# Performance work log

Measured on AMD Instinct MI355X. Metric: run time of the kernel, lower is better.

The kernel has to match this reference:

```python
import jax, jax.numpy as jnp
import numpy as np
from jax import lax

N_CHANNELS = 16
FIRE_RATE = 0.5
ALIVE_THRESH = 0.1


def _perceive_kernel(n_channels):
    sx = jnp.array([[-1., 0., 1.], [-2., 0., 2.], [-1., 0., 1.]], dtype=jnp.float32) / 8.0
    sy = sx.T
    ident = jnp.outer(jnp.array([0., 1., 0.], jnp.float32), jnp.array([0., 1., 0.], jnp.float32))
    base = jnp.stack([ident, sx, sy], axis=0)            # (3,3,3)
    k = jnp.tile(base, (n_channels, 1, 1))[:, None]       # (3n,1,3,3) order: id,sx,sy per channel
    return k


def _maxpool3(a):
    # torch max_pool2d(kernel=3, stride=1, padding=1) with -inf padding
    return lax.reduce_window(a, -jnp.inf, lax.max, (1, 1, 3, 3), (1, 1, 1, 1),
                             ((0, 0), (0, 0), (1, 1), (1, 1)))


def _living(x):
    return _maxpool3(x[:, 3:4]) > ALIVE_THRESH


def setup_inputs() -> dict:
    key = jax.random.key(0)
    k1, k2, k3, k4, k5 = jax.random.split(key, 5)
    B, C, H, W = 32, N_CHANNELS, 256, 256
    HID = 128
    x = jax.random.uniform(k1, (B, C, H, W), dtype=jnp.float32)
    update_rand = jax.random.uniform(k2, (B, 1, H, W), dtype=jnp.float32)
    w1 = jax.random.normal(k3, (HID, 3 * C), dtype=jnp.float32) * 0.1
    b1 = jax.random.normal(k4, (HID,), dtype=jnp.float32) * 0.1
    w2 = jax.random.normal(k5, (C, HID), dtype=jnp.float32) * 0.1
    return {"x": x, "update_rand": update_rand, "w1": w1, "b1": b1, "w2": w2}


def reference(x, update_rand, w1, b1, w2):
    kernel = _perceive_kernel(N_CHANNELS)
    begin_living = _living(x)                                        # (B,1,H,W) bool
    # depthwise perception: groups = n_channels, 3 filters per group
    y = lax.conv_general_dilated(x, kernel, (1, 1), ((1, 1), (1, 1)),
                                 feature_group_count=N_CHANNELS,
                                 dimension_numbers=("NCHW", "OIHW", "NCHW"))  # (B,3C,H,W)
    h = jax.nn.relu(jnp.einsum("bchw,oc->bohw", y, w1) + b1[None, :, None, None])
    dx = jnp.einsum("bhij,oh->boij", h, w2)                          # (B,C,H,W)
    update = (update_rand <= FIRE_RATE).astype(x.dtype)              # (B,1,H,W)
    x_new = x + dx * update
    alive = begin_living & _living(x_new)
    return x_new * alive.astype(x.dtype)
```

## Files before the change

### kernel.cpp

```cpp
#include <hip/hip_runtime.h>

#define CN 16
#define HN 128
#define IMH 256
#define IMW 256
#define HW (IMH * IMW)

typedef __attribute__((ext_vector_type(8))) short short8;
typedef __attribute__((ext_vector_type(4))) float float4v;
typedef __attribute__((ext_vector_type(2))) unsigned int uint2v;
typedef __attribute__((ext_vector_type(4))) unsigned int uint4v;

__device__ __forceinline__ unsigned int f2bf(float f) {
    unsigned int u = __builtin_bit_cast(unsigned int, f);
    u += 0x7FFFu + ((u >> 16) & 1u);
    return u >> 16;
}
__device__ __forceinline__ unsigned int pack2(float a, float b) {
    unsigned int r;
    asm("v_cvt_pk_bf16_f32 %0, %1, %2" : "=v"(r) : "v"(a), "v"(b));
    return r;
}

__global__ void nca_prep(const float* __restrict__ w1, const float* __restrict__ b1,
                         const float* __restrict__ w2,
                         unsigned short* __restrict__ a1f, unsigned short* __restrict__ b2f)
{
    int t = blockIdx.x * 256 + threadIdx.x;
    if (t < 8192) {
        int j = t & 7, lane = (t >> 3) & 63, ks = (t >> 9) & 1, mi = t >> 10;
        int hid = 16 * mi + (lane & 15);
        int k = 32 * ks + 8 * (lane >> 4) + j;
        float v = 0.f;
        if (k < 48) v = w1[hid * 48 + k];
        else if (k == 48) v = b1[hid];
        a1f[t] = (unsigned short)f2bf(v);
    }
    if (t < 2048) {
        int j = t & 7, lane = (t >> 3) & 63, ks = t >> 9;
        b2f[t] = (unsigned short)f2bf(w2[(lane & 15) * HN + 32 * ks + 8 * (lane >> 4) + j]);
    }
}

__global__ __launch_bounds__(256, 4) void nca_mfma(
    const float* __restrict__ x, const float* __restrict__ upd,
    const unsigned short* __restrict__ a1f, const unsigned short* __restrict__ b2f,
    float* __restrict__ out, float* __restrict__ xn3, unsigned char* __restrict__ bm)
{
    __shared__ __align__(16) union {
        float sx[6][16][34];
        unsigned short hb[4][16][128];
    } u;
    __shared__ __align__(16) unsigned short ybuf[128][64];
    __shared__ __align__(16) float xcT[16][128];

    const int b   = blockIdx.z;
    const int i0  = blockIdx.y * 4;
    const int j0  = blockIdx.x * 32;
    const int tid = threadIdx.x;
    const int lane = tid & 63, w = tid >> 6;
    const int l15 = lane & 15, q = lane >> 4;
    const float* xb = x + (size_t)b * CN * HW;

    short8 a1[8][2];
#pragma unroll
    for (int mi = 0; mi < 8; ++mi)
#pragma unroll
        for (int ks = 0; ks < 2; ++ks)
            a1[mi][ks] = *(const short8*)(a1f + ((mi * 2 + ks) * 64 + lane) * 8);
    short8 b2[4];
#pragma unroll
    for (int ks = 0; ks < 4; ++ks)
        b2[ks] = *(const short8*)(b2f + (ks * 64 + lane) * 8);

    const bool interior = (blockIdx.y > 0) & (blockIdx.y < 63) & (blockIdx.x > 0) & (blockIdx.x < 7);
    {
        const int col = tid & 31;
        if (interior) {
            const float* src = xb + (i0 - 1) * IMW + (j0 - 1);
#pragma unroll
            for (int rt = tid >> 5; rt < 96; rt += 8)
                u.sx[rt >> 4][rt & 15][col] = src[(rt & 15) * HW + (rt >> 4) * IMW + col];
            if (tid < 192) {
                int rt = tid >> 1, col2 = 32 + (tid & 1);
                u.sx[rt >> 4][rt & 15][col2] = src[(rt & 15) * HW + (rt >> 4) * IMW + col2];
            }
        } else {
#pragma unroll
            for (int rt = tid >> 5; rt < 96; rt += 8) {
                int rr = rt >> 4, c = rt & 15;
                int gi = i0 + rr - 1, gj = j0 + col - 1;
                float v = 0.f;
                if ((unsigned)gi < IMH && (unsigned)gj < IMW) v = xb[c * HW + gi * IMW + gj];
                u.sx[rr][c][col] = v;
            }
            if (tid < 192) {
                int rt = tid >> 1, col2 = 32 + (tid & 1);
                int rr = rt >> 4, c = rt & 15;
                int gi = i0 + rr - 1, gj = j0 + col2 - 1;
                float v = 0.f;
                if ((unsigned)gi < IMH && (unsigned)gj < IMW) v = xb[c * HW + gi * IMW + gj];
                u.sx[rr][c][col2] = v;
            }
        }
    }
    __syncthreads();

    const int pix = tid & 127;
    const int ty  = pix >> 5, tx = pix & 31;
    const int cb  = (tid >> 7) << 3;
    float v[24];
#pragma unroll
    for (int c8 = 0; c8 < 8; ++c8) {
        const int c = cb + c8;
        float a00 = u.sx[ty][c][tx],     a01 = u.sx[ty][c][tx + 1],     a02 = u.sx[ty][c][tx + 2];
        float a10 = u.sx[ty + 1][c][tx], a11 = u.sx[ty + 1][c][tx + 1], a12 = u.sx[ty + 1][c][tx + 2];
        float a20 = u.sx[ty + 2][c][tx], a21 = u.sx[ty + 2][c][tx + 1], a22 = u.sx[ty + 2][c][tx + 2];
        v[3 * c8]     = a11;
        v[3 * c8 + 1] = ((a02 - a00) + 2.f * (a12 - a10) + (a22 - a20)) * 0.125f;
        v[3 * c8 + 2] = ((a20 - a00) + 2.f * (a21 - a01) + (a22 - a02)) * 0.125f;
        xcT[c][pix ^ ((c & 7) << 2)] = a11;
        if (cb == 0 && c8 == 3) {
            float m0 = fmaxf(fmaxf(fmaxf(a00, a01), fmaxf(a02, a10)),
                             fmaxf(fmaxf(a11, a12), fmaxf(fmaxf(a20, a21), a22)));
            bm[(size_t)b * HW + (i0 + ty) * IMW + (j0 + tx)] = (m0 > 0.1f) ? 1 : 0;
        }
    }
    {
        unsigned int* yrow = (unsigned int*)&ybuf[pix][0];
        const int gbase = (cb >> 3) * 3;
        const int sw = pix & 7;
#pragma unroll
        for (int t = 0; t < 3; ++t) {
            uint4v g;
#pragma unroll
            for (int k = 0; k < 4; ++k) g[k] = pack2(v[8 * t + 2 * k], v[8 * t + 2 * k + 1]);
            *(uint4v*)&yrow[((gbase + t) ^ sw) << 2] = g;
        }
        if (cb == 8) {
            uint4v g6 = {0x3F80u, 0u, 0u, 0u};
            uint4v g7 = {};
            *(uint4v*)&yrow[(6 ^ sw) << 2] = g6;
            *(uint4v*)&yrow[(7 ^ sw) << 2] = g7;
        }
    }
    __syncthreads();

    const float* ub = upd + (size_t)b * HW;
    float* ob = out + (size_t)b * CN * HW;
    float* n3 = xn3 + (size_t)b * HW;
#pragma unroll
    for (int half = 0; half < 2; ++half) {
        const int nt  = 2 * w + half;
        const int row = 16 * nt + l15;
        const unsigned short* yr = &ybuf[row][0];
        const int rsw = row & 7;
        short8 y0 = *(const short8*)(yr + ((q ^ rsw) << 3));
        short8 y1 = *(const short8*)(yr + (((4 + q) ^ rsw) << 3));
        const int hsw = l15 & 7;
#pragma unroll
        for (int mi = 0; mi < 8; ++mi) {
            float4v acc = {};
            acc = __builtin_amdgcn_mfma_f32_16x16x32_bf16(a1[mi][0], y0, acc, 0, 0, 0);
            acc = __builtin_amdgcn_mfma_f32_16x16x32_bf16(a1[mi][1], y1, acc, 0, 0, 0);
            uint2v hp;
            hp[0] = pack2(fmaxf(acc[0], 0.f), fmaxf(acc[1], 0.f));
            hp[1] = pack2(fmaxf(acc[2], 0.f), fmaxf(acc[3], 0.f));
            *(uint2v*)&u.hb[w][l15][(((2 * mi + (q >> 1)) ^ hsw) << 3) + ((q & 1) << 2)] = hp;
        }
        float4v acc2 = {};
#pragma unroll
        for (int ks = 0; ks < 4; ++ks) {
            short8 hf = *(const short8*)&u.hb[w][l15][((4 * ks + q) ^ hsw) << 3];
            acc2 = __builtin_amdgcn_mfma_f32_16x16x32_bf16(hf, b2[ks], acc2, 0, 0, 0);
        }
        const int i  = i0 + (nt >> 1);
        const int jb = j0 + ((nt & 1) << 4) + (q << 2);
        float4v xc4 = *(const float4v*)&xcT[l15][(16 * nt + 4 * q) ^ ((l15 & 7) << 2)];
        float4v u4  = *(const float4v*)(ub + i * IMW + jb);
        float4v o;
#pragma unroll
        for (int r = 0; r < 4; ++r)
            o[r] = fmaf(acc2[r], (u4[r] <= 0.5f) ? 1.f : 0.f, xc4[r]);
        *(float4v*)(ob + l15 * HW + i * IMW + jb) = o;
        if (l15 == 3) *(float4v*)(n3 + i * IMW + jb) = o;
    }
}

__global__ __launch_bounds__(256) void nca_pass2(
    const float* __restrict__ xn3, const unsigned char* __restrict__ bm,
    float* __restrict__ out)
{
    __shared__ float s[10][130];
    const int b  = blockIdx.z;
    const int i0 = blockIdx.y * 8;
    const int j0 = blockIdx.x * 128;
    const int tid = threadIdx.x;
    const float* n3 = xn3 + (size_t)b * HW;

    for (int idx = tid; idx < 10 * 130; idx += 256) {
        int r = idx / 130, c = idx - r * 130;
        int gi = i0 + r - 1, gj = j0 + c - 1;
        s[r][c] = ((unsigned)gi < IMH && (unsigned)gj < IMW) ? n3[gi * IMW + gj] : -1e30f;
    }
    __syncthreads();

    const int c = tid & 127, rh = (tid >> 7) * 4;
    const unsigned char* bmp = bm + (size_t)b * HW + (i0 + rh) * IMW + (j0 + c);
    float* ob = out + (size_t)b * CN * HW;
#pragma unroll
    for (int k = 0; k < 4; ++k) {
        const int r = rh + k;
        float m = fmaxf(fmaxf(fmaxf(s[r][c], s[r][c + 1]), fmaxf(s[r][c + 2], s[r + 1][c])),
                        fmaxf(fmaxf(s[r + 1][c + 1], s[r + 1][c + 2]),
                              fmaxf(fmaxf(s[r + 2][c], s[r + 2][c + 1]), s[r + 2][c + 2])));
        if (!((m > 0.1f) && bmp[k * IMW])) {
            const int i = i0 + r, j = j0 + c;
#pragma unroll
            for (int ch = 0; ch < CN; ++ch)
                ob[ch * HW + i * IMW + j] = 0.f;
        }
    }
}

extern "C" void kernel_launch(void* const* d_in, const int* in_sizes, int n_in,
                              void* d_out, int out_size, void* d_ws, size_t ws_size,
                              hipStream_t stream) {
    const float* x   = (const float*)d_in[0];
    const float* upd = (const float*)d_in[1];
    const float* w1  = (const float*)d_in[2];
    const float* b1  = (const float*)d_in[3];
    const float* w2  = (const float*)d_in[4];
    float* out = (float*)d_out;

    char* ws = (char*)d_ws;
    float* xn3          = (float*)ws;
    unsigned char* bmp  = (unsigned char*)(ws + (8u << 20));
    unsigned short* a1f = (unsigned short*)(ws + (10u << 20));
    unsigned short* b2f = a1f + 8192;

    nca_prep<<<32, 256, 0, stream>>>(w1, b1, w2, a1f, b2f);
    nca_mfma<<<dim3(8, 64, 32), 256, 0, stream>>>(x, upd, a1f, b2f, out, xn3, bmp);
    nca_pass2<<<dim3(2, 32, 32), 256, 0, stream>>>(xn3, bmp, out);
}
```

Measured before the change: 412.6 us.

## Make MFMA kernel persistent over row strips with register-prefetched halo loads

```diff
diff --git a/kernel.cpp b/kernel.cpp
--- a/kernel.cpp
+++ b/kernel.cpp
@@ -55,12 +55,14 @@
     __shared__ __align__(16) float xcT[16][128];
 
     const int b   = blockIdx.z;
-    const int i0  = blockIdx.y * 4;
     const int j0  = blockIdx.x * 32;
     const int tid = threadIdx.x;
     const int lane = tid & 63, w = tid >> 6;
     const int l15 = lane & 15, q = lane >> 4;
     const float* xb = x + (size_t)b * CN * HW;
+    const float* ub = upd + (size_t)b * HW;
+    float* ob = out + (size_t)b * CN * HW;
+    float* n3 = xn3 + (size_t)b * HW;
 
     short8 a1[8][2];
 #pragma unroll
@@ -73,117 +75,144 @@
     for (int ks = 0; ks < 4; ++ks)
         b2[ks] = *(const short8*)(b2f + (ks * 64 + lane) * 8);
 
-    const bool interior = (blockIdx.y > 0) & (blockIdx.y < 63) & (blockIdx.x > 0) & (blockIdx.x < 7);
-    {
-        const int col = tid & 31;
-        if (interior) {
+    const int col    = tid & 31;
+    const int rbase  = tid >> 5;
+    const int ex_rt  = tid >> 1;
+    const int ex_col = 32 + (tid & 1);
+    const bool xin = (blockIdx.x > 0) & (blockIdx.x < 7);
+
+    float sreg[12];
+    float sx1 = 0.f;
+
+    auto issue_stage = [&](int i0) {
+        if (xin && (i0 > 0) && (i0 < 252)) {
             const float* src = xb + (i0 - 1) * IMW + (j0 - 1);
 #pragma unroll
-            for (int rt = tid >> 5; rt < 96; rt += 8)
-                u.sx[rt >> 4][rt & 15][col] = src[(rt & 15) * HW + (rt >> 4) * IMW + col];
-            if (tid < 192) {
-                int rt = tid >> 1, col2 = 32 + (tid & 1);
-                u.sx[rt >> 4][rt & 15][col2] = src[(rt & 15) * HW + (rt >> 4) * IMW + col2];
-            }
+            for (int k = 0; k < 12; ++k) {
+                const int rt = rbase + 8 * k;
+                sreg[k] = src[(rt & 15) * HW + (rt >> 4) * IMW + col];
+            }
+            if (tid < 192) sx1 = src[(ex_rt & 15) * HW + (ex_rt >> 4) * IMW + ex_col];
         } else {
 #pragma unroll
-            for (int rt = tid >> 5; rt < 96; rt += 8) {
-                int rr = rt >> 4, c = rt & 15;
-                int gi = i0 + rr - 1, gj = j0 + col - 1;
+            for (int k = 0; k < 12; ++k) {
+                const int rt = rbase + 8 * k;
+                const int rr = rt >> 4, c = rt & 15;
+                const int gi = i0 + rr - 1, gj = j0 + col - 1;
                 float v = 0.f;
                 if ((unsigned)gi < IMH && (unsigned)gj < IMW) v = xb[c * HW + gi * IMW + gj];
-                u.sx[rr][c][col] = v;
+                sreg[k] = v;
             }
             if (tid < 192) {
-                int rt = tid >> 1, col2 = 32 + (tid & 1);
-                int rr = rt >> 4, c = rt & 15;
-                int gi = i0 + rr - 1, gj = j0 + col2 - 1;
+                const int rr = ex_rt >> 4, c = ex_rt & 15;
+                const int gi = i0 + rr - 1, gj = j0 + ex_col - 1;
                 float v = 0.f;
                 if ((unsigned)gi < IMH && (unsigned)gj < IMW) v = xb[c * HW + gi * IMW + gj];
-                u.sx[rr][c][col2] = v;
-            }
-        }
-    }
-    __syncthreads();
-
-    const int pix = tid & 127;
-    const int ty  = pix >> 5, tx = pix & 31;
-    const int cb  = (tid >> 7) << 3;
-    float v[24];
-#pragma unroll
-    for (int c8 = 0; c8 < 8; ++c8) {
-        const int c = cb + c8;
-        float a00 = u.sx[ty][c][tx],     a01 = u.sx[ty][c][tx + 1],     a02 = u.sx[ty][c][tx + 2];
-        float a10 = u.sx[ty + 1][c][tx], a11 = u.sx[ty + 1][c][tx + 1], a12 = u.sx[ty + 1][c][tx + 2];
-        float a20 = u.sx[ty + 2][c][tx], a21 = u.sx[ty + 2][c][tx + 1], a22 = u.sx[ty + 2][c][tx + 2];
-        v[3 * c8]     = a11;
-        v[3 * c8 + 1] = ((a02 - a00) + 2.f * (a12 - a10) + (a22 - a20)) * 0.125f;
-        v[3 * c8 + 2] = ((a20 - a00) + 2.f * (a21 - a01) + (a22 - a02)) * 0.125f;
-        xcT[c][pix ^ ((c & 7) << 2)] = a11;
-        if (cb == 0 && c8 == 3) {
-            float m0 = fmaxf(fmaxf(fmaxf(a00, a01), fmaxf(a02, a10)),
-                             fmaxf(fmaxf(a11, a12), fmaxf(fmaxf(a20, a21), a22)));
-            bm[(size_t)b * HW + (i0 + ty) * IMW + (j0 + tx)] = (m0 > 0.1f) ? 1 : 0;
-        }
-    }
-    {
-        unsigned int* yrow = (unsigned int*)&ybuf[pix][0];
-        const int gbase = (cb >> 3) * 3;
-        const int sw = pix & 7;
-#pragma unroll
-        for (int t = 0; t < 3; ++t) {
-            uint4v g;
-#pragma unroll
-            for (int k = 0; k < 4; ++k) g[k] = pack2(v[8 * t + 2 * k], v[8 * t + 2 * k + 1]);
-            *(uint4v*)&yrow[((gbase + t) ^ sw) << 2] = g;
-        }
-        if (cb == 8) {
-            uint4v g6 = {0x3F80u, 0u, 0u, 0u};
-            uint4v g7 = {};
-            *(uint4v*)&yrow[(6 ^ sw) << 2] = g6;
-            *(uint4v*)&yrow[(7 ^ sw) << 2] = g7;
-        }
-    }
-    __syncthreads();
-
-    const float* ub = upd + (size_t)b * HW;
-    float* ob = out + (size_t)b * CN * HW;
-    float* n3 = xn3 + (size_t)b * HW;
-#pragma unroll
-    for (int half = 0; half < 2; ++half) {
-        const int nt  = 2 * w + half;
-        const int row = 16 * nt + l15;
-        const unsigned short* yr = &ybuf[row][0];
-        const int rsw = row & 7;
-        short8 y0 = *(const short8*)(yr + ((q ^ rsw) << 3));
-        short8 y1 = *(const short8*)(yr + (((4 + q) ^ rsw) << 3));
-        const int hsw = l15 & 7;
-#pragma unroll
-        for (int mi = 0; mi < 8; ++mi) {
-            float4v acc = {};
-            acc = __builtin_amdgcn_mfma_f32_16x16x32_bf16(a1[mi][0], y0, acc, 0, 0, 0);
-            acc = __builtin_amdgcn_mfma_f32_16x16x32_bf16(a1[mi][1], y1, acc, 0, 0, 0);
-            uint2v hp;
-            hp[0] = pack2(fmaxf(acc[0], 0.f), fmaxf(acc[1], 0.f));
-            hp[1] = pack2(fmaxf(acc[2], 0.f), fmaxf(acc[3], 0.f));
-            *(uint2v*)&u.hb[w][l15][(((2 * mi + (q >> 1)) ^ hsw) << 3) + ((q & 1) << 2)] = hp;
-        }
-        float4v acc2 = {};
-#pragma unroll
-        for (int ks = 0; ks < 4; ++ks) {
-            short8 hf = *(const short8*)&u.hb[w][l15][((4 * ks + q) ^ hsw) << 3];
-            acc2 = __builtin_amdgcn_mfma_f32_16x16x32_bf16(hf, b2[ks], acc2, 0, 0, 0);
-        }
-        const int i  = i0 + (nt >> 1);
-        const int jb = j0 + ((nt & 1) << 4) + (q << 2);
-        float4v xc4 = *(const float4v*)&xcT[l15][(16 * nt + 4 * q) ^ ((l15 & 7) << 2)];
-        float4v u4  = *(const float4v*)(ub + i * IMW + jb);
-        float4v o;
-#pragma unroll
-        for (int r = 0; r < 4; ++r)
-            o[r] = fmaf(acc2[r], (u4[r] <= 0.5f) ? 1.f : 0.f, xc4[r]);
-        *(float4v*)(ob + l15 * HW + i * IMW + jb) = o;
-        if (l15 == 3) *(float4v*)(n3 + i * IMW + jb) = o;
+                sx1 = v;
+            }
+        }
+    };
+
+    issue_stage(blockIdx.y * 32);
+
+#pragma unroll 1
+    for (int it = 0; it < 8; ++it) {
+        const int i0 = blockIdx.y * 32 + it * 4;
+
+#pragma unroll
+        for (int k = 0; k < 12; ++k) {
+            const int rt = rbase + 8 * k;
+            u.sx[rt >> 4][rt & 15][col] = sreg[k];
+        }
+        if (tid < 192) u.sx[ex_rt >> 4][ex_rt & 15][ex_col] = sx1;
+        __syncthreads();
+
+        if (it < 7) issue_stage(i0 + 4);
+
+        float4v u4h[2];
+#pragma unroll
+        for (int half = 0; half < 2; ++half) {
+            const int nt = 2 * w + half;
+            u4h[half] = *(const float4v*)(ub + (i0 + (nt >> 1)) * IMW + j0
+                                          + ((nt & 1) << 4) + (q << 2));
+        }
+
+        const int pix = tid & 127;
+        const int ty  = pix >> 5, tx = pix & 31;
+        const int cb  = (tid >> 7) << 3;
+        float v[24];
+#pragma unroll
+        for (int c8 = 0; c8 < 8; ++c8) {
+            const int c = cb + c8;
+            float a00 = u.sx[ty][c][tx],     a01 = u.sx[ty][c][tx + 1],     a02 = u.sx[ty][c][tx + 2];
+            float a10 = u.sx[ty + 1][c][tx], a11 = u.sx[ty + 1][c][tx + 1], a12 = u.sx[ty + 1][c][tx + 2];
+            float a20 = u.sx[ty + 2][c][tx], a21 = u.sx[ty + 2][c][tx + 1], a22 = u.sx[ty + 2][c][tx + 2];
+            v[3 * c8]     = a11;
+            v[3 * c8 + 1] = ((a02 - a00) + 2.f * (a12 - a10) + (a22 - a20)) * 0.125f;
+            v[3 * c8 + 2] = ((a20 - a00) + 2.f * (a21 - a01) + (a22 - a02)) * 0.125f;
+            xcT[c][pix ^ ((c & 7) << 2)] = a11;
+            if (cb == 0 && c8 == 3) {
+                float m0 = fmaxf(fmaxf(fmaxf(a00, a01), fmaxf(a02, a10)),
+                                 fmaxf(fmaxf(a11, a12), fmaxf(fmaxf(a20, a21), a22)));
+                bm[(size_t)b * HW + (i0 + ty) * IMW + (j0 + tx)] = (m0 > 0.1f) ? 1 : 0;
+            }
+        }
+        {
+            unsigned int* yrow = (unsigned int*)&ybuf[pix][0];
+            const int gbase = (cb >> 3) * 3;
+            const int sw = pix & 7;
+#pragma unroll
+            for (int t = 0; t < 3; ++t) {
+                uint4v g;
+#pragma unroll
+                for (int k = 0; k < 4; ++k) g[k] = pack2(v[8 * t + 2 * k], v[8 * t + 2 * k + 1]);
+                *(uint4v*)&yrow[((gbase + t) ^ sw) << 2] = g;
+            }
+            if (cb == 8) {
+                uint4v g6 = {0x3F80u, 0u, 0u, 0u};
+                uint4v g7 = {};
+                *(uint4v*)&yrow[(6 ^ sw) << 2] = g6;
+                *(uint4v*)&yrow[(7 ^ sw) << 2] = g7;
+            }
+        }
+        __syncthreads();
+
+#pragma unroll
+        for (int half = 0; half < 2; ++half) {
+            const int nt  = 2 * w + half;
+            const int row = 16 * nt + l15;
+            const unsigned short* yr = &ybuf[row][0];
+            const int rsw = row & 7;
+            short8 y0 = *(const short8*)(yr + ((q ^ rsw) << 3));
+            short8 y1 = *(const short8*)(yr + (((4 + q) ^ rsw) << 3));
+            const int hsw = l15 & 7;
+#pragma unroll
+            for (int mi = 0; mi < 8; ++mi) {
+                float4v acc = {};
+                acc = __builtin_amdgcn_mfma_f32_16x16x32_bf16(a1[mi][0], y0, acc, 0, 0, 0);
+                acc = __builtin_amdgcn_mfma_f32_16x16x32_bf16(a1[mi][1], y1, acc, 0, 0, 0);
+                uint2v hp;
+                hp[0] = pack2(fmaxf(acc[0], 0.f), fmaxf(acc[1], 0.f));
+                hp[1] = pack2(fmaxf(acc[2], 0.f), fmaxf(acc[3], 0.f));
+                *(uint2v*)&u.hb[w][l15][(((2 * mi + (q >> 1)) ^ hsw) << 3) + ((q & 1) << 2)] = hp;
+            }
+            float4v acc2 = {};
+#pragma unroll
+            for (int ks = 0; ks < 4; ++ks) {
+                short8 hf = *(const short8*)&u.hb[w][l15][((4 * ks + q) ^ hsw) << 3];
+                acc2 = __builtin_amdgcn_mfma_f32_16x16x32_bf16(hf, b2[ks], acc2, 0, 0, 0);
+            }
+            const int i  = i0 + (nt >> 1);
+            const int jb = j0 + ((nt & 1) << 4) + (q << 2);
+            float4v xc4 = *(const float4v*)&xcT[l15][(16 * nt + 4 * q) ^ ((l15 & 7) << 2)];
+            float4v o;
+#pragma unroll
+            for (int r = 0; r < 4; ++r)
+                o[r] = fmaf(acc2[r], (u4h[half][r] <= 0.5f) ? 1.f : 0.f, xc4[r]);
+            *(float4v*)(ob + l15 * HW + i * IMW + jb) = o;
+            if (l15 == 3) *(float4v*)(n3 + i * IMW + jb) = o;
+        }
+        __syncthreads();
     }
 }
 
@@ -191,34 +220,40 @@
     const float* __restrict__ xn3, const unsigned char* __restrict__ bm,
     float* __restrict__ out)
 {
-    __shared__ float s[10][130];
-    const int b  = blockIdx.z;
-    const int i0 = blockIdx.y * 8;
-    const int j0 = blockIdx.x * 128;
+    __shared__ float s[10][264];
+    const int b   = blockIdx.z;
+    const int i0  = blockIdx.y * 8;
     const int tid = threadIdx.x;
     const float* n3 = xn3 + (size_t)b * HW;
 
-    for (int idx = tid; idx < 10 * 130; idx += 256) {
-        int r = idx / 130, c = idx - r * 130;
-        int gi = i0 + r - 1, gj = j0 + c - 1;
-        s[r][c] = ((unsigned)gi < IMH && (unsigned)gj < IMW) ? n3[gi * IMW + gj] : -1e30f;
-    }
+#pragma unroll
+    for (int t = 0; t < 3; ++t) {
+        const int idx = tid + 256 * t;
+        if (idx < 640) {
+            const int r = idx >> 6, c4 = idx & 63;
+            const int gi = i0 + r - 1;
+            float4v vv;
+            if ((unsigned)gi < IMH) vv = *(const float4v*)(n3 + gi * IMW + 4 * c4);
+            else { vv[0] = vv[1] = vv[2] = vv[3] = -1e30f; }
+            *(float4v*)&s[r][4 + 4 * c4] = vv;
+        }
+    }
+    if (tid < 20) { const int r = tid >> 1; s[r][(tid & 1) ? 260 : 3] = -1e30f; }
     __syncthreads();
 
-    const int c = tid & 127, rh = (tid >> 7) * 4;
-    const unsigned char* bmp = bm + (size_t)b * HW + (i0 + rh) * IMW + (j0 + c);
+    const int c = tid;
+    const unsigned char* bmb = bm + (size_t)b * HW + i0 * IMW + c;
     float* ob = out + (size_t)b * CN * HW;
 #pragma unroll
-    for (int k = 0; k < 4; ++k) {
-        const int r = rh + k;
-        float m = fmaxf(fmaxf(fmaxf(s[r][c], s[r][c + 1]), fmaxf(s[r][c + 2], s[r + 1][c])),
-                        fmaxf(fmaxf(s[r + 1][c + 1], s[r + 1][c + 2]),
-                              fmaxf(fmaxf(s[r + 2][c], s[r + 2][c + 1]), s[r + 2][c + 2])));
-        if (!((m > 0.1f) && bmp[k * IMW])) {
-            const int i = i0 + r, j = j0 + c;
+    for (int r = 0; r < 8; ++r) {
+        float m = fmaxf(fmaxf(fmaxf(s[r][c + 3], s[r][c + 4]), fmaxf(s[r][c + 5], s[r + 1][c + 3])),
+                        fmaxf(fmaxf(s[r + 1][c + 4], s[r + 1][c + 5]),
+                              fmaxf(fmaxf(s[r + 2][c + 3], s[r + 2][c + 4]), s[r + 2][c + 5])));
+        if (!((m > 0.1f) && bmb[r * IMW])) {
+            const int i = i0 + r;
 #pragma unroll
             for (int ch = 0; ch < CN; ++ch)
-                ob[ch * HW + i * IMW + j] = 0.f;
+                ob[ch * HW + i * IMW + c] = 0.f;
         }
     }
 }
@@ -240,6 +275,6 @@
     unsigned short* b2f = a1f + 8192;
 
     nca_prep<<<32, 256, 0, stream>>>(w1, b1, w2, a1f, b2f);
-    nca_mfma<<<dim3(8, 64, 32), 256, 0, stream>>>(x, upd, a1f, b2f, out, xn3, bmp);
-    nca_pass2<<<dim3(2, 32, 32), 256, 0, stream>>>(xn3, bmp, out);
-}
+    nca_mfma<<<dim3(8, 8, 32), 256, 0, stream>>>(x, upd, a1f, b2f, out, xn3, bmp);
+    nca_pass2<<<dim3(1, 32, 32), 256, 0, stream>>>(xn3, bmp, out);
+}
```

Result: slower. 702.8 us, median of 2 (+70.3%).

## Shrink LDS usage in MFMA kernel and widen pass2 tiles with vector loads

Applied to the files above, without the earlier changes.

```diff
diff --git a/kernel.cpp b/kernel.cpp
--- a/kernel.cpp
+++ b/kernel.cpp
@@ -51,8 +51,7 @@
         float sx[6][16][34];
         unsigned short hb[4][16][128];
     } u;
-    __shared__ __align__(16) unsigned short ybuf[128][64];
-    __shared__ __align__(16) float xcT[16][128];
+    __shared__ __align__(16) unsigned short ybuf[128][48];
 
     const int b   = blockIdx.z;
     const int i0  = blockIdx.y * 4;
@@ -119,7 +118,6 @@
         v[3 * c8]     = a11;
         v[3 * c8 + 1] = ((a02 - a00) + 2.f * (a12 - a10) + (a22 - a20)) * 0.125f;
         v[3 * c8 + 2] = ((a20 - a00) + 2.f * (a21 - a01) + (a22 - a02)) * 0.125f;
-        xcT[c][pix ^ ((c & 7) << 2)] = a11;
         if (cb == 0 && c8 == 3) {
             float m0 = fmaxf(fmaxf(fmaxf(a00, a01), fmaxf(a02, a10)),
                              fmaxf(fmaxf(a11, a12), fmaxf(fmaxf(a20, a21), a22)));
@@ -129,19 +127,13 @@
     {
         unsigned int* yrow = (unsigned int*)&ybuf[pix][0];
         const int gbase = (cb >> 3) * 3;
-        const int sw = pix & 7;
+        const int sw = pix & 1;
 #pragma unroll
         for (int t = 0; t < 3; ++t) {
             uint4v g;
 #pragma unroll
             for (int k = 0; k < 4; ++k) g[k] = pack2(v[8 * t + 2 * k], v[8 * t + 2 * k + 1]);
             *(uint4v*)&yrow[((gbase + t) ^ sw) << 2] = g;
-        }
-        if (cb == 8) {
-            uint4v g6 = {0x3F80u, 0u, 0u, 0u};
-            uint4v g7 = {};
-            *(uint4v*)&yrow[(6 ^ sw) << 2] = g6;
-            *(uint4v*)&yrow[(7 ^ sw) << 2] = g7;
         }
     }
     __syncthreads();
@@ -154,9 +146,11 @@
         const int nt  = 2 * w + half;
         const int row = 16 * nt + l15;
         const unsigned short* yr = &ybuf[row][0];
-        const int rsw = row & 7;
+        const int rsw = row & 1;
         short8 y0 = *(const short8*)(yr + ((q ^ rsw) << 3));
-        short8 y1 = *(const short8*)(yr + (((4 + q) ^ rsw) << 3));
+        short8 y1 = {};
+        if (q < 2)      y1 = *(const short8*)(yr + (((4 + q) ^ rsw) << 3));
+        else if (q == 2) y1[0] = (short)0x3F80;
         const int hsw = l15 & 7;
 #pragma unroll
         for (int mi = 0; mi < 8; ++mi) {
@@ -176,7 +170,7 @@
         }
         const int i  = i0 + (nt >> 1);
         const int jb = j0 + ((nt & 1) << 4) + (q << 2);
-        float4v xc4 = *(const float4v*)&xcT[l15][(16 * nt + 4 * q) ^ ((l15 & 7) << 2)];
+        float4v xc4 = *(const float4v*)(xb + (size_t)l15 * HW + i * IMW + jb);
         float4v u4  = *(const float4v*)(ub + i * IMW + jb);
         float4v o;
 #pragma unroll
@@ -191,34 +185,40 @@
     const float* __restrict__ xn3, const unsigned char* __restrict__ bm,
     float* __restrict__ out)
 {
-    __shared__ float s[10][130];
-    const int b  = blockIdx.z;
-    const int i0 = blockIdx.y * 8;
-    const int j0 = blockIdx.x * 128;
+    __shared__ float s[10][264];
+    const int b   = blockIdx.z;
+    const int i0  = blockIdx.y * 8;
     const int tid = threadIdx.x;
     const float* n3 = xn3 + (size_t)b * HW;
 
-    for (int idx = tid; idx < 10 * 130; idx += 256) {
-        int r = idx / 130, c = idx - r * 130;
-        int gi = i0 + r - 1, gj = j0 + c - 1;
-        s[r][c] = ((unsigned)gi < IMH && (unsigned)gj < IMW) ? n3[gi * IMW + gj] : -1e30f;
-    }
+#pragma unroll
+    for (int t = 0; t < 3; ++t) {
+        const int idx = tid + 256 * t;
+        if (idx < 640) {
+            const int r = idx >> 6, c4 = idx & 63;
+            const int gi = i0 + r - 1;
+            float4v vv;
+            if ((unsigned)gi < IMH) vv = *(const float4v*)(n3 + gi * IMW + 4 * c4);
+            else { vv[0] = vv[1] = vv[2] = vv[3] = -1e30f; }
+            *(float4v*)&s[r][4 + 4 * c4] = vv;
+        }
+    }
+    if (tid < 20) { const int r = tid >> 1; s[r][(tid & 1) ? 260 : 3] = -1e30f; }
     __syncthreads();
 
-    const int c = tid & 127, rh = (tid >> 7) * 4;
-    const unsigned char* bmp = bm + (size_t)b * HW + (i0 + rh) * IMW + (j0 + c);
+    const int c = tid;
+    const unsigned char* bmb = bm + (size_t)b * HW + i0 * IMW + c;
     float* ob = out + (size_t)b * CN * HW;
 #pragma unroll
-    for (int k = 0; k < 4; ++k) {
-        const int r = rh + k;
-        float m = fmaxf(fmaxf(fmaxf(s[r][c], s[r][c + 1]), fmaxf(s[r][c + 2], s[r + 1][c])),
-                        fmaxf(fmaxf(s[r + 1][c + 1], s[r + 1][c + 2]),
-                              fmaxf(fmaxf(s[r + 2][c], s[r + 2][c + 1]), s[r + 2][c + 2])));
-        if (!((m > 0.1f) && bmp[k * IMW])) {
-            const int i = i0 + r, j = j0 + c;
+    for (int r = 0; r < 8; ++r) {
+        float m = fmaxf(fmaxf(fmaxf(s[r][c + 3], s[r][c + 4]), fmaxf(s[r][c + 5], s[r + 1][c + 3])),
+                        fmaxf(fmaxf(s[r + 1][c + 4], s[r + 1][c + 5]),
+                              fmaxf(fmaxf(s[r + 2][c + 3], s[r + 2][c + 4]), s[r + 2][c + 5])));
+        if (!((m > 0.1f) && bmb[r * IMW])) {
+            const int i = i0 + r;
 #pragma unroll
             for (int ch = 0; ch < CN; ++ch)
-                ob[ch * HW + i * IMW + j] = 0.f;
+                ob[ch * HW + i * IMW + c] = 0.f;
         }
     }
 }
@@ -241,5 +241,5 @@
 
     nca_prep<<<32, 256, 0, stream>>>(w1, b1, w2, a1f, b2f);
     nca_mfma<<<dim3(8, 64, 32), 256, 0, stream>>>(x, upd, a1f, b2f, out, xn3, bmp);
-    nca_pass2<<<dim3(2, 32, 32), 256, 0, stream>>>(xn3, bmp, out);
-}
+    nca_pass2<<<dim3(1, 32, 32), 256, 0, stream>>>(xn3, bmp, out);
+}
```

After: 421.6 us. 1.02x slower.
